# Kernel tuning notes

Hardware: AMD Instinct MI355X
Metric: run time of the kernel (lower is better)

The kernel has to match this reference:

```python
import jax, jax.numpy as jnp
import numpy as np

N_NODES = 100000
N_EDGES = 1600000
F_IN = 128
HID = 64
N_CLS = 40


def _sage_conv(x, src, dst, Wl, bl, Wr, num_nodes):
    # PyG SAGEConv (aggr='mean', root_weight=True, normalize=False):
    # out = lin_l(mean_{j in N(i)} x_j) + lin_r(x_i)
    msg = x[src]                                              # [E, F] gather
    agg = jax.ops.segment_sum(msg, dst, num_segments=num_nodes)
    deg = jax.ops.segment_sum(jnp.ones_like(dst, dtype=x.dtype), dst,
                              num_segments=num_nodes)
    mean = agg / jnp.maximum(deg, 1.0)[:, None]               # [N, F]
    return mean @ Wl.T + bl + x @ Wr.T


def setup_inputs() -> dict:
    key = jax.random.key(0)
    ks = jax.random.split(key, 16)

    def lin(k, out_d, in_d):
        bound = 1.0 / np.sqrt(in_d)
        return jax.random.uniform(k, (out_d, in_d), jnp.float32, -bound, bound)

    x = jax.random.normal(ks[0], (N_NODES, F_IN), jnp.float32)
    edge_index = jax.random.randint(ks[1], (2, N_EDGES), 0, N_NODES, jnp.int64)

    return {
        "x": x,
        "edge_index": edge_index,
        "W1l": lin(ks[2], HID, F_IN), "b1": jnp.zeros((HID,), jnp.float32),
        "W1r": lin(ks[3], HID, F_IN),
        "W2l": lin(ks[4], HID, HID), "b2": jnp.zeros((HID,), jnp.float32),
        "W2r": lin(ks[5], HID, HID),
        "W3l": lin(ks[6], HID, HID), "b3": jnp.zeros((HID,), jnp.float32),
        "W3r": lin(ks[7], HID, HID),
        "Wout": lin(ks[8], N_CLS, HID),
        "bout": jnp.zeros((N_CLS,), jnp.float32),
    }


def reference(x, edge_index, W1l, b1, W1r, W2l, b2, W2r, W3l, b3, W3r, Wout, bout):
    src, dst = edge_index[0], edge_index[1]
    n = x.shape[0]
    h = _sage_conv(x, src, dst, W1l, b1, W1r, n)
    h = jax.nn.elu(h)
    h = _sage_conv(h, src, dst, W2l, b2, W2r, n)
    h = jax.nn.elu(h)
    h = _sage_conv(h, src, dst, W3l, b3, W3r, n)
    return h @ Wout.T + bout
```

## Files before the change

### kernel.cpp

```cpp
#include <hip/hip_runtime.h>


static inline size_t ws_align(size_t x) { return (x + 511) & ~size_t(511); }

#define MAXBC  104
#define CAPL   96
#define EB_CAP 24576

using frag_ab = __attribute__((ext_vector_type(8))) short;
using f32x4   = __attribute__((ext_vector_type(4))) float;

__device__ inline short f2bf(float f) {
    unsigned u = __builtin_bit_cast(unsigned, f);
    u += 0x7fff + ((u >> 16) & 1);
    return (short)(u >> 16);
}
__device__ inline float b2f(unsigned short h) {
    unsigned u = ((unsigned)h) << 16;
    return __builtin_bit_cast(float, u);
}

__global__ void setup_kernel(const float* __restrict__ W1l, const float* __restrict__ W1r,
                             const float* __restrict__ W2l, const float* __restrict__ W2r,
                             const float* __restrict__ W3l, const float* __restrict__ W3r,
                             const float* __restrict__ Wout,
                             unsigned short* __restrict__ fw, int* __restrict__ bcur) {
    const int idx = blockIdx.x * 256 + threadIdx.x;
    if (blockIdx.x == 0 && threadIdx.x < MAXBC) bcur[threadIdx.x] = 0;
    if (idx >= 36864) return;
    if (idx < 32768) {
        const float* W;
        unsigned short* out;
        int F, rel;
        if (idx < 8192)       { W = W1l; out = fw;        F = 128; rel = idx; }
        else if (idx < 16384) { W = W1r; out = fw + 8192; F = 128; rel = idx - 8192; }
        else {
            const int q = (idx - 16384) >> 12;
            rel = (idx - 16384) & 4095;
            F = 64;
            W = (q == 0) ? W2l : (q == 1) ? W2r : (q == 2) ? W3l : W3r;
            out = fw + 16384 + q * 4096;
        }
        const int k = rel % F;
        const int col = rel / F;
        out[(k >> 3) * 512 + col * 8 + (k & 7)] = (unsigned short)f2bf(W[rel]);
    } else {
        const int rel = idx - 32768;
        const int col = rel / 64;
        const int k = rel % 64;
        const float v = (col < 40) ? Wout[col * 64 + k] : 0.0f;
        fw[32768 + (k >> 3) * 512 + col * 8 + (k & 7)] = (unsigned short)f2bf(v);
    }
}

__global__ void pass1_bin(const int* __restrict__ src, const int* __restrict__ dst,
                          int* __restrict__ bcur, unsigned* __restrict__ ebuf,
                          int nE, int nN, int nbc) {
    __shared__ unsigned lbuf[MAXBC][CAPL];
    __shared__ int bcnt[MAXBC];
    __shared__ int gbase[MAXBC];
    const int t = threadIdx.x;
    const int e0 = blockIdx.x * 4096;
    for (int i = t; i < MAXBC; i += 256) bcnt[i] = 0;
    __syncthreads();
#pragma unroll
    for (int q = 0; q < 16; ++q) {
        const int e = e0 + q * 256 + t;
        if (e < nE) {
            const unsigned d = (unsigned)dst[e];
            const unsigned s = (unsigned)src[e];
            if (d < (unsigned)nN && s < (unsigned)nN) {
                const int cb = (int)(d >> 10);
                const unsigned v = ((d & 1023u) << 17) | s;
                const int pos = atomicAdd(&bcnt[cb], 1);
                if (pos < CAPL) {
                    lbuf[cb][pos] = v;
                } else {
                    const int gp = atomicAdd(&bcur[cb], 1);
                    if (gp < EB_CAP) ebuf[(size_t)cb * EB_CAP + gp] = v;
                }
            }
        }
    }
    __syncthreads();
    for (int b = t; b < nbc; b += 256) {
        const int cnt = min(bcnt[b], CAPL);
        bcnt[b] = cnt;
        gbase[b] = (cnt > 0) ? atomicAdd(&bcur[b], cnt) : 0;
    }
    __syncthreads();
    const int wid = t >> 6, lane = t & 63;
    for (int b = wid; b < nbc; b += 4) {
        const int cnt = bcnt[b];
        const int gb = gbase[b];
        for (int i = lane; i < cnt; i += 64) {
            const int gp = gb + i;
            if (gp < EB_CAP) ebuf[(size_t)b * EB_CAP + gp] = lbuf[b][i];
        }
    }
}

__device__ __forceinline__ void pass2_body(const unsigned* __restrict__ ebuf,
                                           const int* __restrict__ bcur,
                                           int* __restrict__ rowptr, int* __restrict__ csr,
                                           int nN, int nbc, int b) {
    __shared__ int sc[128];
    __shared__ int lcnt[1024];
    __shared__ int lcur[1024];
    __shared__ int sdata[256];
    const int node0 = b << 10;
    const int nloc = min(1024, nN - node0);
    if (nloc <= 0) return;
    const int t = threadIdx.x;

    if (t < 128) sc[t] = (t < nbc) ? min(bcur[t], EB_CAP) : 0;
    __syncthreads();
    for (int off = 1; off < 128; off <<= 1) {
        int add = (t < 128 && t >= off) ? sc[t - off] : 0;
        __syncthreads();
        if (t < 128) sc[t] += add;
        __syncthreads();
    }
    const int cnt  = min(bcur[b], EB_CAP);
    const int base = sc[b] - cnt;
    const unsigned* eb = ebuf + (size_t)b * EB_CAP;

    for (int i = t; i < 1024; i += 256) lcnt[i] = 0;
    __syncthreads();
    for (int i = t; i < cnt; i += 256) atomicAdd(&lcnt[eb[i] >> 17], 1);
    __syncthreads();
    int v[4];
    int tsum = 0;
#pragma unroll
    for (int q = 0; q < 4; ++q) { v[q] = lcnt[t * 4 + q]; tsum += v[q]; }
    sdata[t] = tsum;
    __syncthreads();
    for (int off = 1; off < 256; off <<= 1) {
        int add = (t >= off) ? sdata[t - off] : 0;
        __syncthreads();
        sdata[t] += add;
        __syncthreads();
    }
    int run = sdata[t] - tsum;
#pragma unroll
    for (int q = 0; q < 4; ++q) {
        const int l = t * 4 + q;
        lcur[l] = run;
        if (l < nloc) rowptr[node0 + l] = base + run;
        run += v[q];
    }
    if (b == nbc - 1 && t == 0) rowptr[nN] = base + cnt;
    __syncthreads();
    for (int i = t; i < cnt; i += 256) {
        const unsigned ev = eb[i];
        const int pos = atomicAdd(&lcur[ev >> 17], 1);
        csr[base + pos] = (int)((ev & 0x1FFFFu) << 7);
    }
}

template<int F, bool AF32>
__device__ __forceinline__ void proj_body(const void* __restrict__ Aptr,
                                          const unsigned short* __restrict__ fwl,
                                          const unsigned short* __restrict__ fwr,
                                          const float* __restrict__ bias,
                                          unsigned short* __restrict__ xl,
                                          unsigned short* __restrict__ xr,
                                          int nN, int bid) {
    const int t    = threadIdx.x;
    const int wave = t >> 6;
    const int lane = t & 63;
    const int lg   = lane >> 4;
    const int lr   = lane & 15;
    const int row0 = bid * 64 + wave * 16;

    const float*          Af = (const float*)Aptr;
    const unsigned short* Ab = (const unsigned short*)Aptr;

    f32x4 accl[4] = {};
    f32x4 accr[4] = {};

#pragma unroll
    for (int ks = 0; ks < F / 32; ++ks) {
        const int k0 = ks * 32 + lg * 8;
        frag_ab afr;
        {
            int row = row0 + lr;
            if (row >= nN) row = nN - 1;
            if constexpr (AF32) {
                const float4 f0 = *reinterpret_cast<const float4*>(Af + (size_t)row * F + k0);
                const float4 f1 = *reinterpret_cast<const float4*>(Af + (size_t)row * F + k0 + 4);
                afr[0] = f2bf(f0.x); afr[1] = f2bf(f0.y); afr[2] = f2bf(f0.z); afr[3] = f2bf(f0.w);
                afr[4] = f2bf(f1.x); afr[5] = f2bf(f1.y); afr[6] = f2bf(f1.z); afr[7] = f2bf(f1.w);
            } else {
                afr = *reinterpret_cast<const frag_ab*>(Ab + (size_t)row * F + k0);
            }
        }
        const int ob = (ks * 4 + lg) * 512;
#pragma unroll
        for (int nf = 0; nf < 4; ++nf) {
            const int col = nf * 16 + lr;
            const frag_ab bl = *reinterpret_cast<const frag_ab*>(fwl + ob + col * 8);
            const frag_ab br = *reinterpret_cast<const frag_ab*>(fwr + ob + col * 8);
            accl[nf] = __builtin_amdgcn_mfma_f32_16x16x32_bf16(afr, bl, accl[nf], 0, 0, 0);
            accr[nf] = __builtin_amdgcn_mfma_f32_16x16x32_bf16(afr, br, accr[nf], 0, 0, 0);
        }
    }

#pragma unroll
    for (int nf = 0; nf < 4; ++nf) {
        const int col = nf * 16 + lr;
        const float bv = bias[col];
#pragma unroll
        for (int j = 0; j < 4; ++j) {
            const int row = row0 + lg * 4 + j;
            if (row < nN) {
                xl[(size_t)row * 64 + col] = (unsigned short)f2bf(accl[nf][j]);
                xr[(size_t)row * 64 + col] = (unsigned short)f2bf(accr[nf][j] + bv);
            }
        }
    }
}

__global__ void fused_p2_proj1(const unsigned* __restrict__ ebuf,
                               const int* __restrict__ bcur,
                               int* __restrict__ rowptr, int* __restrict__ csr,
                               int nN, int nbc,
                               const float* __restrict__ x,
                               const unsigned short* __restrict__ fwl,
                               const unsigned short* __restrict__ fwr,
                               const float* __restrict__ bias,
                               unsigned short* __restrict__ xl,
                               unsigned short* __restrict__ xr) {
    if ((int)blockIdx.x < nbc)
        pass2_body(ebuf, bcur, rowptr, csr, nN, nbc, blockIdx.x);
    else
        proj_body<128, true>(x, fwl, fwr, bias, xl, xr, nN, blockIdx.x - nbc);
}

template<int F, bool AF32>
__global__ void proj2_mfma(const void* __restrict__ Aptr,
                           const unsigned short* __restrict__ fwl,
                           const unsigned short* __restrict__ fwr,
                           const float* __restrict__ bias,
                           unsigned short* __restrict__ xl,
                           unsigned short* __restrict__ xr,
                           int nN) {
    proj_body<F, AF32>(Aptr, fwl, fwr, bias, xl, xr, nN, blockIdx.x);
}

template<bool DOELU>
__global__ void gather_kernel(const unsigned short* __restrict__ xl,
                              const unsigned short* __restrict__ xr,
                              const int* __restrict__ rowptr, const int* __restrict__ csr,
                              unsigned short* __restrict__ outp, int nN, int nE) {
    const int node = blockIdx.x * (blockDim.x >> 6) + (threadIdx.x >> 6);
    if (node >= nN) return;
    const int lane = threadIdx.x & 63;
    int b = rowptr[node];
    int e = rowptr[node + 1];
    b = max(0, min(b, nE));
    e = max(b, min(e, nE));
    b = __builtin_amdgcn_readfirstlane(b);
    e = __builtin_amdgcn_readfirstlane(e);
    const float d = (float)(e - b);
    const char* xlb = (const char*)xl + (lane << 1);

    float acc = 0.f;
    int i = b;
    for (; i + 16 <= e; i += 16) {
        unsigned short v[16];
#pragma unroll
        for (int j = 0; j < 16; ++j) {
            const unsigned s = (unsigned)csr[i + j];
            v[j] = *(const unsigned short*)(xlb + s);
        }
#pragma unroll
        for (int j = 0; j < 16; ++j) acc += b2f(v[j]);
    }
    if (i < e) {
        const int lim = e - i;
        unsigned short v[16];
#pragma unroll
        for (int j = 0; j < 16; ++j) {
            const unsigned s = (unsigned)csr[i + min(j, lim - 1)];
            v[j] = *(const unsigned short*)(xlb + s);
        }
#pragma unroll
        for (int j = 0; j < 16; ++j) acc += (j < lim) ? b2f(v[j]) : 0.f;
    }

    float vout = acc / fmaxf(d, 1.0f) + b2f(xr[(size_t)node * 64 + lane]);
    if (DOELU) vout = vout > 0.f ? vout : expm1f(vout);
    outp[(size_t)node * 64 + lane] = (unsigned short)f2bf(vout);
}

__global__ void head_mfma(const unsigned short* __restrict__ A,
                          const unsigned short* __restrict__ fwo,
                          const float* __restrict__ bias,
                          float* __restrict__ out, int nN) {
    const int t    = threadIdx.x;
    const int wave = t >> 6;
    const int lane = t & 63;
    const int lg   = lane >> 4;
    const int lr   = lane & 15;
    const int row0 = blockIdx.x * 64 + wave * 16;

    f32x4 acc[3] = {};

#pragma unroll
    for (int ks = 0; ks < 2; ++ks) {
        const int k0 = ks * 32 + lg * 8;
        frag_ab afr;
        {
            int row = row0 + lr;
            if (row >= nN) row = nN - 1;
            afr = *reinterpret_cast<const frag_ab*>(A + (size_t)row * 64 + k0);
        }
        const int ob = (ks * 4 + lg) * 512;
#pragma unroll
        for (int nf = 0; nf < 3; ++nf) {
            const int col = nf * 16 + lr;
            const frag_ab bo = *reinterpret_cast<const frag_ab*>(fwo + ob + col * 8);
            acc[nf] = __builtin_amdgcn_mfma_f32_16x16x32_bf16(afr, bo, acc[nf], 0, 0, 0);
        }
    }

#pragma unroll
    for (int nf = 0; nf < 3; ++nf) {
        const int col = nf * 16 + lr;
        if (col >= 40) continue;
        const float bv = bias[col];
#pragma unroll
        for (int j = 0; j < 4; ++j) {
            const int row = row0 + lg * 4 + j;
            if (row < nN)
                out[(size_t)row * 40 + col] = acc[nf][j] + bv;
        }
    }
}


extern "C" void kernel_launch(void* const* d_in, const int* in_sizes, int n_in,
                              void* d_out, int out_size, void* d_ws, size_t ws_size,
                              hipStream_t stream) {
    const float* x    = (const float*)d_in[0];
    const int*   ei   = (const int*)d_in[1];
    const float* W1l  = (const float*)d_in[2];
    const float* b1   = (const float*)d_in[3];
    const float* W1r  = (const float*)d_in[4];
    const float* W2l  = (const float*)d_in[5];
    const float* b2   = (const float*)d_in[6];
    const float* W2r  = (const float*)d_in[7];
    const float* W3l  = (const float*)d_in[8];
    const float* b3   = (const float*)d_in[9];
    const float* W3r  = (const float*)d_in[10];
    const float* Wout = (const float*)d_in[11];
    const float* bout = (const float*)d_in[12];

    const int N = in_sizes[0] / 128;
    const int E = in_sizes[1] / 2;
    const int* src  = ei;
    const int* dstA = ei + E;
    const int nbc = (N + 1023) >> 10;
    const int nbP1 = (E + 4095) / 4096;

    char* ws = (char*)d_ws;
    size_t o = 0;
    int* bcur    = (int*)(ws + o); o += ws_align((size_t)MAXBC * 4);
    int* rowptr  = (int*)(ws + o); o += ws_align((size_t)(N + 1) * 4);
    int* csr     = (int*)(ws + o); o += ws_align((size_t)E * 4);
    unsigned* ebuf = (unsigned*)(ws + o); o += ws_align((size_t)MAXBC * EB_CAP * 4);
    unsigned short* fw  = (unsigned short*)(ws + o); o += ws_align((size_t)36864 * 2);
    unsigned short* xl  = (unsigned short*)(ws + o); o += ws_align((size_t)N * 64 * 2);
    unsigned short* xr  = (unsigned short*)(ws + o); o += ws_align((size_t)N * 64 * 2);
    unsigned short* hAb = (unsigned short*)(ws + o); o += ws_align((size_t)N * 64 * 2);
    unsigned short* hBb = (unsigned short*)(ws + o); o += ws_align((size_t)N * 64 * 2);
    unsigned short* h3b = (unsigned short*)(ws + o); o += ws_align((size_t)N * 64 * 2);
    float* outp = (float*)d_out;

    const int projGrid = (N + 63) / 64;
    const int gatherGrid = (N + 3) / 4;

    const unsigned short* fw1l = fw;
    const unsigned short* fw1r = fw + 8192;
    const unsigned short* fw2l = fw + 16384;
    const unsigned short* fw2r = fw + 16384 + 4096;
    const unsigned short* fw3l = fw + 16384 + 8192;
    const unsigned short* fw3r = fw + 16384 + 12288;
    const unsigned short* fwo  = fw + 32768;

    setup_kernel<<<144, 256, 0, stream>>>(W1l, W1r, W2l, W2r, W3l, W3r, Wout, fw, bcur);

    pass1_bin<<<nbP1, 256, 0, stream>>>(src, dstA, bcur, ebuf, E, N, nbc);

    fused_p2_proj1<<<nbc + projGrid, 256, 0, stream>>>(
        ebuf, bcur, rowptr, csr, N, nbc,
        x, fw1l, fw1r, b1, xl, xr);

    gather_kernel<true><<<gatherGrid, 256, 0, stream>>>(xl, xr, rowptr, csr, hAb, N, E);

    proj2_mfma<64, false><<<projGrid, 256, 0, stream>>>(hAb, fw2l, fw2r, b2, xl, xr, N);
    gather_kernel<true><<<gatherGrid, 256, 0, stream>>>(xl, xr, rowptr, csr, hBb, N, E);

    proj2_mfma<64, false><<<projGrid, 256, 0, stream>>>(hBb, fw3l, fw3r, b3, xl, xr, N);
    gather_kernel<false><<<gatherGrid, 256, 0, stream>>>(xl, xr, rowptr, csr, h3b, N, E);

    head_mfma<<<projGrid, 256, 0, stream>>>(h3b, fwo, bout, outp, N);
}
```

Baseline: 239.4 us.

## Split projected features into 16-column planes and gather each plane separately

The projection now writes xl as four column-major planes of 16 bf16 features per node, and the CSR stores byte offsets scaled for 32-byte rows. The gather runs four passes, one per plane, and each wave handles four edges at a time (16 lanes per edge), then reduces across lanes with shuffles. The aim is a smaller working set per pass so random neighbour rows stay in cache, with more edge-level parallelism per wave. The cost is four times as many blocks re-reading rowptr/csr, partially idle lanes in the epilogue, and 32-byte scattered accesses that use memory transactions less efficiently.

Measured after the change: 719.5 us. 3.01x slower.

```diff
diff --git a/kernel.cpp b/kernel.cpp
--- a/kernel.cpp
+++ b/kernel.cpp
@@ -154,7 +154,7 @@
     for (int i = t; i < cnt; i += 256) {
         const unsigned ev = eb[i];
         const int pos = atomicAdd(&lcur[ev >> 17], 1);
-        csr[base + pos] = (int)((ev & 0x1FFFFu) << 7);
+        csr[base + pos] = (int)((ev & 0x1FFFFu) << 5);
     }
 }
 
@@ -210,11 +210,12 @@
     for (int nf = 0; nf < 4; ++nf) {
         const int col = nf * 16 + lr;
         const float bv = bias[col];
+        unsigned short* xlq = xl + (size_t)nf * nN * 16;
 #pragma unroll
         for (int j = 0; j < 4; ++j) {
             const int row = row0 + lg * 4 + j;
             if (row < nN) {
-                xl[(size_t)row * 64 + col] = (unsigned short)f2bf(accl[nf][j]);
+                xlq[(size_t)row * 16 + lr] = (unsigned short)f2bf(accl[nf][j]);
                 xr[(size_t)row * 64 + col] = (unsigned short)f2bf(accr[nf][j] + bv);
             }
         }
@@ -252,10 +253,15 @@
 __global__ void gather_kernel(const unsigned short* __restrict__ xl,
                               const unsigned short* __restrict__ xr,
                               const int* __restrict__ rowptr, const int* __restrict__ csr,
-                              unsigned short* __restrict__ outp, int nN, int nE) {
-    const int node = blockIdx.x * (blockDim.x >> 6) + (threadIdx.x >> 6);
+                              unsigned short* __restrict__ outp,
+                              int nN, int nE, int nodeBlocks) {
+    const int pass = blockIdx.x / nodeBlocks;
+    const int nb   = blockIdx.x - pass * nodeBlocks;
+    const int node = nb * 4 + (threadIdx.x >> 6);
     if (node >= nN) return;
     const int lane = threadIdx.x & 63;
+    const int es = lane >> 4;
+    const int f  = lane & 15;
     int b = rowptr[node];
     int e = rowptr[node + 1];
     b = max(0, min(b, nE));
@@ -263,35 +269,34 @@
     b = __builtin_amdgcn_readfirstlane(b);
     e = __builtin_amdgcn_readfirstlane(e);
     const float d = (float)(e - b);
-    const char* xlb = (const char*)xl + (lane << 1);
+    const char* xq = (const char*)xl + (size_t)pass * ((size_t)nN * 32) + (f << 1);
 
     float acc = 0.f;
-    int i = b;
-    for (; i + 16 <= e; i += 16) {
-        unsigned short v[16];
-#pragma unroll
-        for (int j = 0; j < 16; ++j) {
-            const unsigned s = (unsigned)csr[i + j];
-            v[j] = *(const unsigned short*)(xlb + s);
-        }
-#pragma unroll
-        for (int j = 0; j < 16; ++j) acc += b2f(v[j]);
-    }
-    if (i < e) {
-        const int lim = e - i;
-        unsigned short v[16];
-#pragma unroll
-        for (int j = 0; j < 16; ++j) {
-            const unsigned s = (unsigned)csr[i + min(j, lim - 1)];
-            v[j] = *(const unsigned short*)(xlb + s);
-        }
-#pragma unroll
-        for (int j = 0; j < 16; ++j) acc += (j < lim) ? b2f(v[j]) : 0.f;
-    }
-
-    float vout = acc / fmaxf(d, 1.0f) + b2f(xr[(size_t)node * 64 + lane]);
-    if (DOELU) vout = vout > 0.f ? vout : expm1f(vout);
-    outp[(size_t)node * 64 + lane] = (unsigned short)f2bf(vout);
+    for (int i = b; i < e; i += 32) {
+        unsigned short v[8];
+        int idx[8];
+#pragma unroll
+        for (int g = 0; g < 8; ++g) {
+            idx[g] = i + g * 4 + es;
+            const int ic = min(idx[g], e - 1);
+            const unsigned s = (unsigned)csr[ic];
+            v[g] = *(const unsigned short*)(xq + s);
+        }
+#pragma unroll
+        for (int g = 0; g < 8; ++g)
+            acc += (idx[g] < e) ? b2f(v[g]) : 0.f;
+    }
+    acc += __shfl_xor(acc, 16);
+    acc += __shfl_xor(acc, 32);
+
+    if (es == 0) {
+        const int col = pass * 16 + f;
+        const unsigned short xru = __builtin_nontemporal_load(&xr[(size_t)node * 64 + col]);
+        float vout = acc / fmaxf(d, 1.0f) + b2f(xru);
+        if (DOELU) vout = vout > 0.f ? vout : expm1f(vout);
+        __builtin_nontemporal_store((unsigned short)f2bf(vout),
+                                    &outp[(size_t)node * 64 + col]);
+    }
 }
 
 __global__ void head_mfma(const unsigned short* __restrict__ A,
@@ -379,7 +384,8 @@
     float* outp = (float*)d_out;
 
     const int projGrid = (N + 63) / 64;
-    const int gatherGrid = (N + 3) / 4;
+    const int nodeBlocks = (N + 3) / 4;
+    const int gatherGrid = 4 * nodeBlocks;
 
     const unsigned short* fw1l = fw;
     const unsigned short* fw1r = fw + 8192;
@@ -397,13 +403,13 @@
         ebuf, bcur, rowptr, csr, N, nbc,
         x, fw1l, fw1r, b1, xl, xr);
 
-    gather_kernel<true><<<gatherGrid, 256, 0, stream>>>(xl, xr, rowptr, csr, hAb, N, E);
+    gather_kernel<true><<<gatherGrid, 256, 0, stream>>>(xl, xr, rowptr, csr, hAb, N, E, nodeBlocks);
 
     proj2_mfma<64, false><<<projGrid, 256, 0, stream>>>(hAb, fw2l, fw2r, b2, xl, xr, N);
-    gather_kernel<true><<<gatherGrid, 256, 0, stream>>>(xl, xr, rowptr, csr, hBb, N, E);
+    gather_kernel<true><<<gatherGrid, 256, 0, stream>>>(xl, xr, rowptr, csr, hBb, N, E, nodeBlocks);
 
     proj2_mfma<64, false><<<projGrid, 256, 0, stream>>>(hBb, fw3l, fw3r, b3, xl, xr, N);
-    gather_kernel<false><<<gatherGrid, 256, 0, stream>>>(xl, xr, rowptr, csr, h3b, N, E);
+    gather_kernel<false><<<gatherGrid, 256, 0, stream>>>(xl, xr, rowptr, csr, h3b, N, E, nodeBlocks);
 
     head_mfma<<<projGrid, 256, 0, stream>>>(h3b, fwo, bout, outp, N);
 }
```
